# Kernel optimization log

Measured on AMD Instinct MI355X. Metric: run time of the kernel, lower is better.

## Reference

```python
import jax, jax.numpy as jnp
import numpy as np


def setup_inputs() -> dict:
    key = jax.random.key(0)
    k1, k2, k3, k4, k5 = jax.random.split(key, 5)
    B, T, R, H = 64, 256, 49, 1024  # batch, caption len, regions (7x7), hidden
    V = jax.random.normal(k1, (B, R, H), dtype=jnp.float32)
    h_t = jax.random.normal(k2, (B, T, H), dtype=jnp.float32)
    Wv = jax.random.normal(k3, (R, H), dtype=jnp.float32) * (1.0 / np.sqrt(H))
    Wg = jax.random.normal(k4, (R, H), dtype=jnp.float32) * (1.0 / np.sqrt(H))
    Wh = jax.random.normal(k5, (1, R), dtype=jnp.float32) * (1.0 / np.sqrt(R))
    return {"V": V, "h_t": h_t, "Wv": Wv, "Wg": Wg, "Wh": Wh}


def reference(V, h_t, Wv, Wg, Wh):
    # content_v: [B,1,R,R] + [B,T,1,R] -> [B,T,R,R]
    cv = jnp.einsum('brh,kh->brk', V, Wv)      # [B, R, R]
    cg = jnp.einsum('bth,kh->btk', h_t, Wg)    # [B, T, R]
    content_v = cv[:, None, :, :] + cg[:, :, None, :]  # [B, T, R, R]
    # z_t = affine_h(tanh(content_v)) squeezed -> [B, T, R]
    z_t = jnp.einsum('btrk,k->btr', jnp.tanh(content_v), Wh[0])
    alpha_t = jax.nn.softmax(z_t, axis=-1)     # [B, T, R]
    c_t = jnp.einsum('btr,brh->bth', alpha_t, V)  # [B, T, H]
    return (c_t, alpha_t)
```

## Files before the change

### kernel.cpp

```cpp
#include <hip/hip_runtime.h>
#include <hip/hip_bf16.h>
#include <math.h>
#include <stdint.h>


typedef __attribute__((ext_vector_type(8))) short bf16x8;
typedef __attribute__((ext_vector_type(4))) float floatx4;

static __device__ __forceinline__ bf16x8 pack8(float4 a, float4 b) {
    union { __hip_bfloat162 h[4]; bf16x8 v; } u;
    u.h[0] = __float22bfloat162_rn(make_float2(a.x, a.y));
    u.h[1] = __float22bfloat162_rn(make_float2(a.z, a.w));
    u.h[2] = __float22bfloat162_rn(make_float2(b.x, b.y));
    u.h[3] = __float22bfloat162_rn(make_float2(b.z, b.w));
    return u.v;
}

static __device__ __forceinline__ unsigned short f2bf_bits(float f) {
    union { __hip_bfloat16 h; unsigned short u; } c;
    c.h = __float2bfloat16(f);
    return c.u;
}

__global__ __launch_bounds__(256) void gemm_mfma_tr(const float* __restrict__ Av,
                                                    const float* __restrict__ Ag,
                                                    const float* __restrict__ Wv,
                                                    const float* __restrict__ Wg,
                                                    float* __restrict__ Cv,
                                                    float* __restrict__ Cg,
                                                    unsigned short* __restrict__ vT) {
    __shared__ __align__(16) char smem[49 * 132 * 4];
    const int bid = blockIdx.x;
    const int tid = threadIdx.x;

    if (bid >= 610) {
        float* Ts = (float*)smem;
        const int tb = bid - 610;
        const int b = tb >> 3;
        const int h0 = (tb & 7) * 128;
        for (int i = tid; i < 49 * 32; i += 256) {
            const int r = i >> 5, hq = i & 31;
            *(float4*)(Ts + r * 132 + hq * 4) =
                *(const float4*)(Av + ((size_t)b * 49 + r) * 1024 + h0 + hq * 4);
        }
        __syncthreads();
        const int h = tid & 127;
        const int half = tid >> 7;
        float f[32];
#pragma unroll
        for (int j = 0; j < 32; ++j) {
            const int r = half * 32 + j;
            f[j] = (r < 49) ? Ts[r * 132 + h] : 0.f;
        }
        const size_t rowbase = ((size_t)b * 1024 + h0 + h) * 64;
#pragma unroll
        for (int o2 = 0; o2 < 4; ++o2) {
            const int o = half * 4 + o2;
            bf16x8 v = pack8(make_float4(f[o2*8+0], f[o2*8+1], f[o2*8+2], f[o2*8+3]),
                             make_float4(f[o2*8+4], f[o2*8+5], f[o2*8+6], f[o2*8+7]));
            *(bf16x8*)(vT + rowbase + (size_t)((o ^ (h & 7)) * 8)) = v;
        }
        return;
    }

    short* As = (short*)smem;
    short* Ws = (short*)(smem + 4096);
    const float* A; const float* W; float* C; int m0;
    if (bid < 98) { A = Av; W = Wv; C = Cv; m0 = bid * 32; }
    else          { A = Ag; W = Wg; C = Cg; m0 = (bid - 98) * 32; }

    const int wave = tid >> 6, lane = tid & 63;
    const int quad = lane >> 4, l16 = lane & 15;
    const int mb = (wave & 1) * 16;
    const int nb = (wave >> 1) * 32;

    floatx4 acc[2] = {};

    const int arow = tid >> 3, ag = tid & 7;
    const int wrow = tid >> 2, wq = tid & 3;
    const float* aptr = A + (size_t)(m0 + arow) * 1024 + ag * 8;
    const bool wvalid = wrow < 49;
    const float* wptr = W + (size_t)wrow * 1024 + wq * 16;

    float4 a0 = *(const float4*)(aptr);
    float4 a1 = *(const float4*)(aptr + 4);
    float4 w0 = make_float4(0.f,0.f,0.f,0.f), w1 = w0, w2 = w0, w3 = w0;
    if (wvalid) {
        w0 = *(const float4*)(wptr);
        w1 = *(const float4*)(wptr + 4);
        w2 = *(const float4*)(wptr + 8);
        w3 = *(const float4*)(wptr + 12);
    }

    for (int kc = 0; kc < 1024; kc += 64) {
        __syncthreads();
        *(bf16x8*)(As + arow * 64 + (ag ^ (arow & 7)) * 8) = pack8(a0, a1);
        *(bf16x8*)(Ws + wrow * 64 + ((wq * 2) ^ (wrow & 7)) * 8) = pack8(w0, w1);
        *(bf16x8*)(Ws + wrow * 64 + ((wq * 2 + 1) ^ (wrow & 7)) * 8) = pack8(w2, w3);
        __syncthreads();
        if (kc < 960) {
            a0 = *(const float4*)(aptr + kc + 64);
            a1 = *(const float4*)(aptr + kc + 68);
            if (wvalid) {
                w0 = *(const float4*)(wptr + kc + 64);
                w1 = *(const float4*)(wptr + kc + 68);
                w2 = *(const float4*)(wptr + kc + 72);
                w3 = *(const float4*)(wptr + kc + 76);
            }
        }
#pragma unroll
        for (int s = 0; s < 2; ++s) {
            const int am = mb + l16;
            bf16x8 af = *(const bf16x8*)(As + am * 64 + (((s << 2) + quad) ^ (am & 7)) * 8);
#pragma unroll
            for (int nt = 0; nt < 2; ++nt) {
                const int wn = nb + nt * 16 + l16;
                bf16x8 bf = *(const bf16x8*)(Ws + wn * 64 + (((s << 2) + quad) ^ (wn & 7)) * 8);
                acc[nt] = __builtin_amdgcn_mfma_f32_16x16x32_bf16(af, bf, acc[nt], 0, 0, 0);
            }
        }
    }

#pragma unroll
    for (int nt = 0; nt < 2; ++nt) {
        const int n = nb + nt * 16 + l16;
        if (n < 49) {
#pragma unroll
            for (int r = 0; r < 4; ++r) {
                const int m = m0 + mb + quad * 4 + r;
                C[(size_t)m * 49 + n] = acc[nt][r];
            }
        }
    }
}

__global__ __launch_bounds__(256) void zsoftmax(const float* __restrict__ cv,
                                                const float* __restrict__ cg,
                                                const float* __restrict__ Wh,
                                                float* __restrict__ alpha,
                                                unsigned short* __restrict__ a16) {
    const int b = blockIdx.x >> 4;
    const int t0 = (blockIdx.x & 15) * 16;
    __shared__ __align__(16) float cvl[49 * 52];
    __shared__ __align__(16) float cgl[16 * 52];
    __shared__ __align__(16) float whl[52];

    const int tid = threadIdx.x;
    for (int i = tid; i < 49 * 49; i += 256) {
        int r = i / 49, k = i - r * 49;
        cvl[r * 52 + k] = cv[(size_t)b * 2401 + i];
    }
    for (int i = tid; i < 16 * 49; i += 256) {
        int t = i / 49, k = i - t * 49;
        cgl[t * 52 + k] = cg[((size_t)b * 256 + t0) * 49 + i];
    }
    if (tid < 52) whl[tid] = (tid < 49) ? Wh[tid] : 0.f;
    __syncthreads();

    const int wave = tid >> 6;
    const int lane = tid & 63;
    const float4* cvr = (const float4*)(cvl + lane * 52);
    const float4* wh4 = (const float4*)whl;

    for (int i = 0; i < 4; ++i) {
        const int tl = wave * 4 + i;
        float z = -INFINITY;
        if (lane < 49) {
            const float4* cgr = (const float4*)(cgl + tl * 52);
            float s = 0.f;
#pragma unroll 4
            for (int kk = 0; kk < 12; ++kk) {
                float4 x = cvr[kk], g = cgr[kk], w = wh4[kk];
                float r0 = __builtin_amdgcn_rcpf(__expf(2.f * (x.x + g.x)) + 1.f);
                float r1 = __builtin_amdgcn_rcpf(__expf(2.f * (x.y + g.y)) + 1.f);
                float r2 = __builtin_amdgcn_rcpf(__expf(2.f * (x.z + g.z)) + 1.f);
                float r3 = __builtin_amdgcn_rcpf(__expf(2.f * (x.w + g.w)) + 1.f);
                s = fmaf(1.f - 2.f * r0, w.x, s);
                s = fmaf(1.f - 2.f * r1, w.y, s);
                s = fmaf(1.f - 2.f * r2, w.z, s);
                s = fmaf(1.f - 2.f * r3, w.w, s);
            }
            {
                float x = cvl[lane * 52 + 48] + cgl[tl * 52 + 48];
                float r0 = __builtin_amdgcn_rcpf(__expf(2.f * x) + 1.f);
                s = fmaf(1.f - 2.f * r0, whl[48], s);
            }
            z = s;
        }
        float m = z;
        for (int off = 32; off; off >>= 1) m = fmaxf(m, __shfl_xor(m, off));
        float p = (lane < 49) ? __expf(z - m) : 0.f;
        float sum = p;
        for (int off = 32; off; off >>= 1) sum += __shfl_xor(sum, off);
        const float val = p * __builtin_amdgcn_rcpf(sum);

        const size_t grow = (size_t)b * 256 + t0 + tl;
        if (lane < 49) alpha[grow * 49 + lane] = val;
        const int pos = (((lane >> 3) ^ (tl & 7)) << 3) | (lane & 7);
        a16[grow * 64 + pos] = f2bf_bits(val);
    }
}

__global__ __launch_bounds__(256) void ct_mfma(const unsigned short* __restrict__ a16,
                                               const unsigned short* __restrict__ vT,
                                               float* __restrict__ C) {
    const int bid = blockIdx.x;
    const int b = bid >> 5;
    const int t0 = ((bid >> 3) & 3) * 64;
    const int h0 = (bid & 7) * 128;

    __shared__ __align__(16) short Al[64 * 64];
    __shared__ __align__(16) short Vl[128 * 64];

    const int tid = threadIdx.x;
    {
        const bf16x8* src = (const bf16x8*)(a16 + ((size_t)b * 256 + t0) * 64);
        bf16x8* dst = (bf16x8*)Al;
#pragma unroll
        for (int p = 0; p < 2; ++p) dst[tid + p * 256] = src[tid + p * 256];
    }
    {
        const bf16x8* src = (const bf16x8*)(vT + ((size_t)b * 1024 + h0) * 64);
        bf16x8* dst = (bf16x8*)Vl;
#pragma unroll
        for (int p = 0; p < 4; ++p) dst[tid + p * 256] = src[tid + p * 256];
    }
    __syncthreads();

    const int wave = tid >> 6, lane = tid & 63;
    const int quad = lane >> 4, l16 = lane & 15;
    const int tb = (wave & 1) * 32;
    const int hb = (wave >> 1) * 64;

    floatx4 acc[2][4] = {};
#pragma unroll
    for (int kc = 0; kc < 2; ++kc) {
        bf16x8 af[2];
#pragma unroll
        for (int ms = 0; ms < 2; ++ms) {
            const int row = tb + ms * 16 + l16;
            af[ms] = *(const bf16x8*)(Al + row * 64 + (((kc << 2) + quad) ^ (row & 7)) * 8);
        }
#pragma unroll
        for (int ns = 0; ns < 4; ++ns) {
            const int row = hb + ns * 16 + l16;
            bf16x8 bf = *(const bf16x8*)(Vl + row * 64 + (((kc << 2) + quad) ^ (row & 7)) * 8);
#pragma unroll
            for (int ms = 0; ms < 2; ++ms)
                acc[ms][ns] = __builtin_amdgcn_mfma_f32_16x16x32_bf16(af[ms], bf, acc[ms][ns], 0, 0, 0);
        }
    }

#pragma unroll
    for (int ms = 0; ms < 2; ++ms) {
        const int t = t0 + tb + ms * 16 + quad * 4;
#pragma unroll
        for (int ns = 0; ns < 4; ++ns) {
            const int h = h0 + hb + ns * 16 + l16;
#pragma unroll
            for (int r = 0; r < 4; ++r)
                C[((size_t)b * 256 + t + r) * 1024 + h] = acc[ms][ns][r];
        }
    }
}

extern "C" void kernel_launch(void* const* d_in, const int* in_sizes, int n_in,
                              void* d_out, int out_size, void* d_ws, size_t ws_size,
                              hipStream_t stream) {
    const float* V   = (const float*)d_in[0];
    const float* h_t = (const float*)d_in[1];
    const float* Wv  = (const float*)d_in[2];
    const float* Wg  = (const float*)d_in[3];
    const float* Wh  = (const float*)d_in[4];

    float* c_t   = (float*)d_out;
    float* alpha = (float*)d_out + 16777216;

    float* cv = (float*)d_ws;
    float* cg = cv + 153664;
    unsigned short* a16 = (unsigned short*)((char*)d_ws + 3825920);
    unsigned short* vT  = a16 + 16384 * 64;

    gemm_mfma_tr<<<610 + 512, 256, 0, stream>>>(V, h_t, Wv, Wg, cv, cg, vT);
    zsoftmax<<<1024, 256, 0, stream>>>(cv, cg, Wh, alpha, a16);
    ct_mfma<<<2048, 256, 0, stream>>>(a16, vT, c_t);
}
```

Baseline: 175.0 us.

## Halve GEMM M-tile, double-buffer LDS, and split V transpose into more blocks

The projection GEMM now uses 16-row M tiles, so it launches twice as many blocks, and each wave owns one 16-column N slice. Shared memory is double-buffered with register prefetch two K-steps ahead, which cuts the loop to a single barrier per step. The V-transpose blocks now cover 64 columns each, so there are twice as many of them. The aim is higher occupancy and better overlap of global loads with MFMA work, at the cost of more redundant W loads per block and more launched blocks.

```diff
diff --git a/kernel.cpp b/kernel.cpp
--- a/kernel.cpp
+++ b/kernel.cpp
@@ -5,6 +5,7 @@
 
 
 typedef __attribute__((ext_vector_type(8))) short bf16x8;
+typedef __attribute__((ext_vector_type(4))) short bf16x4;
 typedef __attribute__((ext_vector_type(4))) float floatx4;
 
 static __device__ __forceinline__ bf16x8 pack8(float4 a, float4 b) {
@@ -16,6 +17,13 @@
     return u.v;
 }
 
+static __device__ __forceinline__ bf16x4 pack4(float4 a) {
+    union { __hip_bfloat162 h[2]; bf16x4 v; } u;
+    u.h[0] = __float22bfloat162_rn(make_float2(a.x, a.y));
+    u.h[1] = __float22bfloat162_rn(make_float2(a.z, a.w));
+    return u.v;
+}
+
 static __device__ __forceinline__ unsigned short f2bf_bits(float f) {
     union { __hip_bfloat16 h; unsigned short u; } c;
     c.h = __float2bfloat16(f);
@@ -29,33 +37,33 @@
                                                     float* __restrict__ Cv,
                                                     float* __restrict__ Cg,
                                                     unsigned short* __restrict__ vT) {
-    __shared__ __align__(16) char smem[49 * 132 * 4];
+    __shared__ __align__(16) char smem[20480];
     const int bid = blockIdx.x;
     const int tid = threadIdx.x;
 
-    if (bid >= 610) {
+    if (bid >= 1220) {
         float* Ts = (float*)smem;
-        const int tb = bid - 610;
-        const int b = tb >> 3;
-        const int h0 = (tb & 7) * 128;
-        for (int i = tid; i < 49 * 32; i += 256) {
-            const int r = i >> 5, hq = i & 31;
-            *(float4*)(Ts + r * 132 + hq * 4) =
+        const int tb = bid - 1220;
+        const int b = tb >> 4;
+        const int h0 = (tb & 15) * 64;
+        for (int i = tid; i < 49 * 16; i += 256) {
+            const int r = i >> 4, hq = i & 15;
+            *(float4*)(Ts + r * 68 + hq * 4) =
                 *(const float4*)(Av + ((size_t)b * 49 + r) * 1024 + h0 + hq * 4);
         }
         __syncthreads();
-        const int h = tid & 127;
-        const int half = tid >> 7;
-        float f[32];
-#pragma unroll
-        for (int j = 0; j < 32; ++j) {
-            const int r = half * 32 + j;
-            f[j] = (r < 49) ? Ts[r * 132 + h] : 0.f;
+        const int h = tid & 63;
+        const int grp = tid >> 6;
+        float f[16];
+#pragma unroll
+        for (int j = 0; j < 16; ++j) {
+            const int r = grp * 16 + j;
+            f[j] = (r < 49) ? Ts[r * 68 + h] : 0.f;
         }
         const size_t rowbase = ((size_t)b * 1024 + h0 + h) * 64;
 #pragma unroll
-        for (int o2 = 0; o2 < 4; ++o2) {
-            const int o = half * 4 + o2;
+        for (int o2 = 0; o2 < 2; ++o2) {
+            const int o = grp * 2 + o2;
             bf16x8 v = pack8(make_float4(f[o2*8+0], f[o2*8+1], f[o2*8+2], f[o2*8+3]),
                              make_float4(f[o2*8+4], f[o2*8+5], f[o2*8+6], f[o2*8+7]));
             *(bf16x8*)(vT + rowbase + (size_t)((o ^ (h & 7)) * 8)) = v;
@@ -66,70 +74,86 @@
     short* As = (short*)smem;
     short* Ws = (short*)(smem + 4096);
     const float* A; const float* W; float* C; int m0;
-    if (bid < 98) { A = Av; W = Wv; C = Cv; m0 = bid * 32; }
-    else          { A = Ag; W = Wg; C = Cg; m0 = (bid - 98) * 32; }
+    if (bid < 196) { A = Av; W = Wv; C = Cv; m0 = bid * 16; }
+    else           { A = Ag; W = Wg; C = Cg; m0 = (bid - 196) * 16; }
 
     const int wave = tid >> 6, lane = tid & 63;
     const int quad = lane >> 4, l16 = lane & 15;
-    const int mb = (wave & 1) * 16;
-    const int nb = (wave >> 1) * 32;
-
-    floatx4 acc[2] = {};
-
-    const int arow = tid >> 3, ag = tid & 7;
+    const int nb = wave * 16;
+
+    floatx4 acc = {};
+
+    const int arow = tid >> 4, ag = tid & 15;
     const int wrow = tid >> 2, wq = tid & 3;
-    const float* aptr = A + (size_t)(m0 + arow) * 1024 + ag * 8;
+    const float* aptr = A + (size_t)(m0 + arow) * 1024 + ag * 4;
     const bool wvalid = wrow < 49;
     const float* wptr = W + (size_t)wrow * 1024 + wq * 16;
-
-    float4 a0 = *(const float4*)(aptr);
-    float4 a1 = *(const float4*)(aptr + 4);
-    float4 w0 = make_float4(0.f,0.f,0.f,0.f), w1 = w0, w2 = w0, w3 = w0;
+    short* adst = As + arow * 64 + (((ag >> 1) ^ (arow & 7)) * 8) + (ag & 1) * 4;
+    short* wdst0 = Ws + wrow * 64;
+
+    float4 ra[2];
+    float4 rw[2][4];
+    const float4 fz = make_float4(0.f, 0.f, 0.f, 0.f);
+
+    ra[0] = *(const float4*)(aptr);
     if (wvalid) {
-        w0 = *(const float4*)(wptr);
-        w1 = *(const float4*)(wptr + 4);
-        w2 = *(const float4*)(wptr + 8);
-        w3 = *(const float4*)(wptr + 12);
-    }
-
-    for (int kc = 0; kc < 1024; kc += 64) {
+        rw[0][0] = *(const float4*)(wptr);
+        rw[0][1] = *(const float4*)(wptr + 4);
+        rw[0][2] = *(const float4*)(wptr + 8);
+        rw[0][3] = *(const float4*)(wptr + 12);
+    } else { rw[0][0] = rw[0][1] = rw[0][2] = rw[0][3] = fz; }
+    *(bf16x4*)(adst) = pack4(ra[0]);
+    *(bf16x8*)(wdst0 + (((wq * 2)     ^ (wrow & 7)) * 8)) = pack8(rw[0][0], rw[0][1]);
+    *(bf16x8*)(wdst0 + (((wq * 2 + 1) ^ (wrow & 7)) * 8)) = pack8(rw[0][2], rw[0][3]);
+    ra[1] = *(const float4*)(aptr + 64);
+    if (wvalid) {
+        rw[1][0] = *(const float4*)(wptr + 64);
+        rw[1][1] = *(const float4*)(wptr + 68);
+        rw[1][2] = *(const float4*)(wptr + 72);
+        rw[1][3] = *(const float4*)(wptr + 76);
+    } else { rw[1][0] = rw[1][1] = rw[1][2] = rw[1][3] = fz; }
+    __syncthreads();
+
+#pragma unroll
+    for (int kc = 0; kc < 16; ++kc) {
+        const int cur = kc & 1;
+        const int curA = cur * 1024, curW = cur * 4096;
+        if (kc < 14) {
+            const int off = (kc + 2) * 64;
+            ra[cur] = *(const float4*)(aptr + off);
+            if (wvalid) {
+                rw[cur][0] = *(const float4*)(wptr + off);
+                rw[cur][1] = *(const float4*)(wptr + off + 4);
+                rw[cur][2] = *(const float4*)(wptr + off + 8);
+                rw[cur][3] = *(const float4*)(wptr + off + 12);
+            }
+        }
+        {
+            const int am = l16;
+            const int wn = nb + l16;
+            bf16x8 af0 = *(const bf16x8*)(As + curA + am * 64 + ((quad       ^ (am & 7)) * 8));
+            bf16x8 af1 = *(const bf16x8*)(As + curA + am * 64 + (((4 + quad) ^ (am & 7)) * 8));
+            bf16x8 bf0 = *(const bf16x8*)(Ws + curW + wn * 64 + ((quad       ^ (wn & 7)) * 8));
+            bf16x8 bf1 = *(const bf16x8*)(Ws + curW + wn * 64 + (((4 + quad) ^ (wn & 7)) * 8));
+            acc = __builtin_amdgcn_mfma_f32_16x16x32_bf16(af0, bf0, acc, 0, 0, 0);
+            acc = __builtin_amdgcn_mfma_f32_16x16x32_bf16(af1, bf1, acc, 0, 0, 0);
+        }
+        if (kc < 15) {
+            const int nxt = cur ^ 1;
+            const int nA = nxt * 1024, nW = nxt * 4096;
+            *(bf16x4*)(adst + nA) = pack4(ra[nxt]);
+            *(bf16x8*)(wdst0 + nW + (((wq * 2)     ^ (wrow & 7)) * 8)) = pack8(rw[nxt][0], rw[nxt][1]);
+            *(bf16x8*)(wdst0 + nW + (((wq * 2 + 1) ^ (wrow & 7)) * 8)) = pack8(rw[nxt][2], rw[nxt][3]);
+        }
         __syncthreads();
-        *(bf16x8*)(As + arow * 64 + (ag ^ (arow & 7)) * 8) = pack8(a0, a1);
-        *(bf16x8*)(Ws + wrow * 64 + ((wq * 2) ^ (wrow & 7)) * 8) = pack8(w0, w1);
-        *(bf16x8*)(Ws + wrow * 64 + ((wq * 2 + 1) ^ (wrow & 7)) * 8) = pack8(w2, w3);
-        __syncthreads();
-        if (kc < 960) {
-            a0 = *(const float4*)(aptr + kc + 64);
-            a1 = *(const float4*)(aptr + kc + 68);
-            if (wvalid) {
-                w0 = *(const float4*)(wptr + kc + 64);
-                w1 = *(const float4*)(wptr + kc + 68);
-                w2 = *(const float4*)(wptr + kc + 72);
-                w3 = *(const float4*)(wptr + kc + 76);
-            }
-        }
-#pragma unroll
-        for (int s = 0; s < 2; ++s) {
-            const int am = mb + l16;
-            bf16x8 af = *(const bf16x8*)(As + am * 64 + (((s << 2) + quad) ^ (am & 7)) * 8);
-#pragma unroll
-            for (int nt = 0; nt < 2; ++nt) {
-                const int wn = nb + nt * 16 + l16;
-                bf16x8 bf = *(const bf16x8*)(Ws + wn * 64 + (((s << 2) + quad) ^ (wn & 7)) * 8);
-                acc[nt] = __builtin_amdgcn_mfma_f32_16x16x32_bf16(af, bf, acc[nt], 0, 0, 0);
-            }
-        }
-    }
-
-#pragma unroll
-    for (int nt = 0; nt < 2; ++nt) {
-        const int n = nb + nt * 16 + l16;
-        if (n < 49) {
-#pragma unroll
-            for (int r = 0; r < 4; ++r) {
-                const int m = m0 + mb + quad * 4 + r;
-                C[(size_t)m * 49 + n] = acc[nt][r];
-            }
+    }
+
+    const int n = nb + l16;
+    if (n < 49) {
+#pragma unroll
+        for (int r = 0; r < 4; ++r) {
+            const int m = m0 + quad * 4 + r;
+            C[(size_t)m * 49 + n] = acc[r];
         }
     }
 }
@@ -281,7 +305,7 @@
     unsigned short* a16 = (unsigned short*)((char*)d_ws + 3825920);
     unsigned short* vT  = a16 + 16384 * 64;
 
-    gemm_mfma_tr<<<610 + 512, 256, 0, stream>>>(V, h_t, Wv, Wg, cv, cg, vT);
+    gemm_mfma_tr<<<196 + 1024 + 1024, 256, 0, stream>>>(V, h_t, Wv, Wg, cv, cg, vT);
     zsoftmax<<<1024, 256, 0, stream>>>(cv, cg, Wh, alpha, a16);
     ct_mfma<<<2048, 256, 0, stream>>>(a16, vT, c_t);
 }
```

Result: slower. 183.9 us (+5.1%).
